# Kernel optimization log

Hardware: AMD Instinct MI355X
Metric: run time of the kernel (lower is better)

Reference implementation:

```python
import jax, jax.numpy as jnp
import numpy as np

N_NODES = 100000
N_EDGES = 4000000
IN_DIM = 3
HID = 8
EPS = 1e-5


def _layer_norm(h, g, b):
    m = jnp.mean(h, axis=-1, keepdims=True)
    v = jnp.mean(jnp.square(h - m), axis=-1, keepdims=True)
    return (h - m) * jax.lax.rsqrt(v + EPS) * g + b


def setup_inputs() -> dict:
    key = jax.random.key(0)
    ks = jax.random.split(key, 10)
    x = jax.random.normal(ks[0], (N_NODES, IN_DIM), dtype=jnp.float32)
    edge_index = jax.random.randint(ks[1], (2, N_EDGES), 0, N_NODES, dtype=jnp.int64)

    def lin(k, fan_in, fan_out):
        bound = 1.0 / np.sqrt(fan_in)
        kw, kb = jax.random.split(k)
        W = jax.random.uniform(kw, (fan_in, fan_out), jnp.float32, -bound, bound)
        b = jax.random.uniform(kb, (fan_out,), jnp.float32, -bound, bound)
        return W, b

    W0, b0 = lin(ks[2], 2 * IN_DIM, HID)
    W1, b1 = lin(ks[3], HID, HID)
    W2, b2 = lin(ks[4], HID, HID)
    W3, b3 = lin(ks[5], HID, 1)
    g0 = jnp.ones((HID,), jnp.float32); be0 = jnp.zeros((HID,), jnp.float32)
    g1 = jnp.ones((HID,), jnp.float32); be1 = jnp.zeros((HID,), jnp.float32)
    g2 = jnp.ones((HID,), jnp.float32); be2 = jnp.zeros((HID,), jnp.float32)
    return {"x": x, "edge_index": edge_index,
            "W0": W0, "b0": b0, "g0": g0, "be0": be0,
            "W1": W1, "b1": b1, "g1": g1, "be1": be1,
            "W2": W2, "b2": b2, "g2": g2, "be2": be2,
            "W3": W3, "b3": b3}


def reference(x, edge_index, W0, b0, g0, be0, W1, b1, g1, be1, W2, b2, g2, be2, W3, b3):
    start, end = edge_index[0], edge_index[1]
    # [E, 2*IN_DIM] gathered edge inputs
    e = jnp.concatenate([x[start], x[end]], axis=1)
    h = jnp.tanh(_layer_norm(e @ W0 + b0, g0, be0))
    h = jnp.tanh(_layer_norm(h @ W1 + b1, g1, be1))
    h = jnp.tanh(_layer_norm(h @ W2 + b2, g2, be2))
    out = (h @ W3 + b3).squeeze(-1)  # [E]
    return out
```

## Files before the change

kernel.cpp:

```cpp
#include <hip/hip_runtime.h>

typedef _Float16 h2 __attribute__((ext_vector_type(2)));
typedef float f4v __attribute__((ext_vector_type(4)));
typedef f4v f4u __attribute__((aligned(4)));

#define N_EDGES 4000000
#define HID 8
#define NPT 4
#define TWO_LOG2E 2.8853900817779268f
#define LN_EPS 1e-5f

#define O_GC0 0
#define O_BC0 8
#define O_GC1 16
#define O_BC1 24
#define O_GC2 32
#define O_BC2 40
#define O_B1  48
#define O_B2  56
#define O_B3  64
#define O_W1P 72
#define O_W2P 104
#define O_W3P 136
#define O_W0C 144
#define O_B0C 192

#if __has_builtin(__builtin_amdgcn_fdot2)
#define FDOT2(a, b, c) __builtin_amdgcn_fdot2((a), (b), (c), false)
#else
#define FDOT2(a, b, c) ((float)(a)[0] * (float)(b)[0] + ((float)(a)[1] * (float)(b)[1] + (c)))
#endif

__global__ void prep_kernel(
    const float* __restrict__ W0, const float* __restrict__ b0,
    const float* __restrict__ g0, const float* __restrict__ be0,
    const float* __restrict__ W1, const float* __restrict__ b1,
    const float* __restrict__ g1, const float* __restrict__ be1,
    const float* __restrict__ W2, const float* __restrict__ b2,
    const float* __restrict__ g2, const float* __restrict__ be2,
    const float* __restrict__ W3, const float* __restrict__ b3,
    float* __restrict__ ws)
{
    if (threadIdx.x != 0) return;
    uint* wsu = reinterpret_cast<uint*>(ws);
    for (int j = 0; j < 8; ++j) {
        ws[O_GC0 + j] = g0[j] * TWO_LOG2E;  ws[O_BC0 + j] = be0[j] * TWO_LOG2E;
        ws[O_GC1 + j] = g1[j] * TWO_LOG2E;  ws[O_BC1 + j] = be1[j] * TWO_LOG2E;
        ws[O_GC2 + j] = g2[j] * TWO_LOG2E;  ws[O_BC2 + j] = be2[j] * TWO_LOG2E;
    }
    {
        float bm = 0.f;
        for (int j = 0; j < 8; ++j) bm += b0[j];
        bm *= 0.125f;
        for (int j = 0; j < 8; ++j) ws[O_B0C + j] = b0[j] - bm;
        for (int k = 0; k < 6; ++k) {
            float rm = 0.f;
            for (int j = 0; j < 8; ++j) rm += W0[k * 8 + j];
            rm *= 0.125f;
            for (int j = 0; j < 8; ++j) ws[O_W0C + k * 8 + j] = W0[k * 8 + j] - rm;
        }
    }
    const float* Ws[2] = {W1, W2};
    const float* bs[2] = {b1, b2};
    const int    wo[2] = {O_W1P, O_W2P};
    const int    bo[2] = {O_B1, O_B2};
    for (int L = 0; L < 2; ++L) {
        const float* W = Ws[L];
        float Wc[64];
        for (int k = 0; k < 8; ++k) {
            float rm = 0.f;
            for (int j = 0; j < 8; ++j) rm += W[k * 8 + j];
            rm *= 0.125f;
            for (int j = 0; j < 8; ++j) Wc[k * 8 + j] = -2.f * (W[k * 8 + j] - rm);
        }
        for (int k = 0; k < 8; ++k) {
            float m = 0.f;
            for (int j = 0; j < 8; ++j) m += (float)(_Float16)Wc[k * 8 + j];
            m *= 0.125f;
            for (int j = 0; j < 8; ++j) Wc[k * 8 + j] -= m;
        }
        for (int j = 0; j < 8; ++j)
            for (int q = 0; q < 4; ++q) {
                h2 v;
                v[0] = (_Float16)Wc[(2 * q) * 8 + j];
                v[1] = (_Float16)Wc[(2 * q + 1) * 8 + j];
                wsu[wo[L] + j * 4 + q] = __builtin_bit_cast(uint, v);
            }
        float mb = 0.f, tot = 0.f;
        for (int j = 0; j < 8; ++j) mb += bs[L][j];
        for (int i = 0; i < 64; ++i) tot += W[i];
        for (int j = 0; j < 8; ++j) {
            float cs = 0.f;
            for (int k = 0; k < 8; ++k) cs += W[k * 8 + j];
            ws[bo[L] + j] = bs[L][j] + cs - mb * 0.125f - tot * 0.125f;
        }
    }
    {
        float s = 0.f;
        for (int k = 0; k < 8; ++k) s += W3[k];
        ws[O_B3] = b3[0] + s;
        for (int q = 0; q < 4; ++q) {
            h2 v;
            v[0] = (_Float16)(-2.f * W3[2 * q]);
            v[1] = (_Float16)(-2.f * W3[2 * q + 1]);
            wsu[O_W3P + q] = __builtin_bit_cast(uint, v);
        }
    }
}

template<int N>
__device__ __forceinline__ void ln_pack(const float (&z)[N][HID],
                                        const float* __restrict__ gc,
                                        const float* __restrict__ bc,
                                        h2 (&p)[N][4]) {
    float r[N];
#pragma unroll
    for (int e = 0; e < N; ++e) {
        float va = 0.f;
#pragma unroll
        for (int j = 0; j < HID; ++j) va = __builtin_fmaf(z[e][j], z[e][j], va);
        r[e] = __builtin_amdgcn_rsqf(__builtin_fmaf(va, 0.125f, LN_EPS));
    }
    float e1[N][HID];
#pragma unroll
    for (int j = 0; j < HID; ++j) {
        const float gcj = gc[j], bcj = bc[j];
#pragma unroll
        for (int e = 0; e < N; ++e) {
            const float y = __builtin_fmaf(z[e][j], r[e] * gcj, bcj);
            e1[e][j] = __builtin_amdgcn_exp2f(y) + 1.0f;
        }
    }
#pragma unroll
    for (int q = 0; q < 4; ++q)
#pragma unroll
        for (int e = 0; e < N; ++e) {
            const float a = e1[e][2 * q], b = e1[e][2 * q + 1];
            const float pr = __builtin_amdgcn_rcpf(a * b);
            p[e][q] = __builtin_bit_cast(h2,
                __builtin_amdgcn_cvt_pkrtz(b * pr, a * pr));
        }
}

template<int N>
__device__ __forceinline__ void lin8_dot(const h2 (&p)[N][4],
                                         const uint* __restrict__ wp,
                                         const float* __restrict__ b,
                                         float (&zo)[N][HID]) {
#pragma unroll
    for (int j = 0; j < HID; ++j) {
        const float bj = b[j];
        const h2 w0 = __builtin_bit_cast(h2, wp[j * 4 + 0]);
        const h2 w1 = __builtin_bit_cast(h2, wp[j * 4 + 1]);
        const h2 w2 = __builtin_bit_cast(h2, wp[j * 4 + 2]);
        const h2 w3 = __builtin_bit_cast(h2, wp[j * 4 + 3]);
#pragma unroll
        for (int e = 0; e < N; ++e) {
            float acc = FDOT2(p[e][0], w0, bj);
            acc = FDOT2(p[e][1], w1, acc);
            acc = FDOT2(p[e][2], w2, acc);
            zo[e][j] = FDOT2(p[e][3], w3, acc);
        }
    }
}

__global__ __launch_bounds__(256) void edge_mlp_kernel(
    const float* __restrict__ x,
    const int*   __restrict__ ei,
    const float* __restrict__ ws,
    float* __restrict__ out)
{
    const int t = blockIdx.x * blockDim.x + threadIdx.x;
    const int base = t * NPT;
    if (base >= N_EDGES) return;

    const uint* wsu = reinterpret_cast<const uint*>(ws);
    const int4 sv = *reinterpret_cast<const int4*>(ei + base);
    const int4 dv = *reinterpret_cast<const int4*>(ei + N_EDGES + base);
    const uint si[NPT] = {(uint)sv.x, (uint)sv.y, (uint)sv.z, (uint)sv.w};
    const uint di[NPT] = {(uint)dv.x, (uint)dv.y, (uint)dv.z, (uint)dv.w};

    f4u vs[NPT], vd[NPT];
#pragma unroll
    for (int e = 0; e < NPT; ++e) {
        vs[e] = *reinterpret_cast<const f4u*>(x + (size_t)(si[e] * 3u));
        vd[e] = *reinterpret_cast<const f4u*>(x + (size_t)(di[e] * 3u));
    }

    float z[NPT][HID];
#pragma unroll
    for (int j = 0; j < HID; ++j) {
        const float w0 = ws[O_W0C + 0 * 8 + j], w1 = ws[O_W0C + 1 * 8 + j],
                    w2 = ws[O_W0C + 2 * 8 + j], w3 = ws[O_W0C + 3 * 8 + j],
                    w4 = ws[O_W0C + 4 * 8 + j], w5 = ws[O_W0C + 5 * 8 + j];
        const float bb = ws[O_B0C + j];
#pragma unroll
        for (int e = 0; e < NPT; ++e) {
            float a = __builtin_fmaf(vs[e][0], w0, bb);
            a = __builtin_fmaf(vs[e][1], w1, a);
            a = __builtin_fmaf(vs[e][2], w2, a);
            a = __builtin_fmaf(vd[e][0], w3, a);
            a = __builtin_fmaf(vd[e][1], w4, a);
            z[e][j] = __builtin_fmaf(vd[e][2], w5, a);
        }
    }

    h2 p[NPT][4];
    ln_pack<NPT>(z, ws + O_GC0, ws + O_BC0, p);
    lin8_dot<NPT>(p, wsu + O_W1P, ws + O_B1, z);
    ln_pack<NPT>(z, ws + O_GC1, ws + O_BC1, p);
    lin8_dot<NPT>(p, wsu + O_W2P, ws + O_B2, z);
    ln_pack<NPT>(z, ws + O_GC2, ws + O_BC2, p);

    const h2 w30 = __builtin_bit_cast(h2, wsu[O_W3P + 0]);
    const h2 w31 = __builtin_bit_cast(h2, wsu[O_W3P + 1]);
    const h2 w32 = __builtin_bit_cast(h2, wsu[O_W3P + 2]);
    const h2 w33 = __builtin_bit_cast(h2, wsu[O_W3P + 3]);
    const float bb3 = ws[O_B3];
    float o[NPT];
#pragma unroll
    for (int e = 0; e < NPT; ++e) {
        float acc = FDOT2(p[e][0], w30, bb3);
        acc = FDOT2(p[e][1], w31, acc);
        acc = FDOT2(p[e][2], w32, acc);
        o[e] = FDOT2(p[e][3], w33, acc);
    }

    *reinterpret_cast<float4*>(out + base) = make_float4(o[0], o[1], o[2], o[3]);
}

extern "C" void kernel_launch(void* const* d_in, const int* in_sizes, int n_in,
                              void* d_out, int out_size, void* d_ws, size_t ws_size,
                              hipStream_t stream) {
    const float* x   = (const float*)d_in[0];
    const int*   ei  = (const int*)d_in[1];
    const float* W0  = (const float*)d_in[2];
    const float* b0  = (const float*)d_in[3];
    const float* g0  = (const float*)d_in[4];
    const float* be0 = (const float*)d_in[5];
    const float* W1  = (const float*)d_in[6];
    const float* b1  = (const float*)d_in[7];
    const float* g1  = (const float*)d_in[8];
    const float* be1 = (const float*)d_in[9];
    const float* W2  = (const float*)d_in[10];
    const float* b2  = (const float*)d_in[11];
    const float* g2  = (const float*)d_in[12];
    const float* be2 = (const float*)d_in[13];
    const float* W3  = (const float*)d_in[14];
    const float* b3  = (const float*)d_in[15];
    float* out = (float*)d_out;
    float* ws  = (float*)d_ws;

    prep_kernel<<<1, 64, 0, stream>>>(W0, b0, g0, be0, W1, b1, g1, be1,
                                      W2, b2, g2, be2, W3, b3, ws);

    const int nthreads = N_EDGES / NPT;
    const int blocks = (nthreads + 255) / 256;
    edge_mlp_kernel<<<blocks, 256, 0, stream>>>(x, ei, ws, out);
}
```

Before: 55.22 us.

## Pack node features to fp16 table and use fdot2 for first layer

The prep kernel now writes a compact 8-byte fp16 copy of each node's features into the workspace, and parallelizes the weight preprocessing across threads. The edge kernel gathers from this packed table instead of 12-16 byte fp32 rows, and computes the first linear layer with fp16 dot2 instructions using packed, zero-padded W0. This is meant to cut gather bandwidth and first-layer ALU work, at the cost of an extra per-call node conversion pass and lower input precision. A fallback path keeps fp32 gathers with conversion when the workspace is too small.

```diff
diff --git a/kernel.cpp b/kernel.cpp
--- a/kernel.cpp
+++ b/kernel.cpp
@@ -1,10 +1,9 @@
 #include <hip/hip_runtime.h>
 
 typedef _Float16 h2 __attribute__((ext_vector_type(2)));
-typedef float f4v __attribute__((ext_vector_type(4)));
-typedef f4v f4u __attribute__((aligned(4)));
 
 #define N_EDGES 4000000
+#define N_NODES 100000
 #define HID 8
 #define NPT 4
 #define TWO_LOG2E 2.8853900817779268f
@@ -22,8 +21,10 @@
 #define O_W1P 72
 #define O_W2P 104
 #define O_W3P 136
-#define O_W0C 144
-#define O_B0C 192
+#define O_W0P 144
+#define O_B0C 176
+#define O_XH  256
+#define WS_FLOATS_NEEDED (256 + 2 * N_NODES)
 
 #if __has_builtin(__builtin_amdgcn_fdot2)
 #define FDOT2(a, b, c) __builtin_amdgcn_fdot2((a), (b), (c), false)
@@ -31,7 +32,42 @@
 #define FDOT2(a, b, c) ((float)(a)[0] * (float)(b)[0] + ((float)(a)[1] * (float)(b)[1] + (c)))
 #endif
 
+__device__ void prep_hidden_layer(const float* __restrict__ W,
+                                  const float* __restrict__ b,
+                                  float* __restrict__ ws, uint* __restrict__ wsu,
+                                  int wofs, int bofs) {
+    float Wc[64];
+    for (int k = 0; k < 8; ++k) {
+        float rm = 0.f;
+        for (int j = 0; j < 8; ++j) rm += W[k * 8 + j];
+        rm *= 0.125f;
+        for (int j = 0; j < 8; ++j) Wc[k * 8 + j] = -2.f * (W[k * 8 + j] - rm);
+    }
+    for (int k = 0; k < 8; ++k) {
+        float m = 0.f;
+        for (int j = 0; j < 8; ++j) m += (float)(_Float16)Wc[k * 8 + j];
+        m *= 0.125f;
+        for (int j = 0; j < 8; ++j) Wc[k * 8 + j] -= m;
+    }
+    for (int j = 0; j < 8; ++j)
+        for (int q = 0; q < 4; ++q) {
+            h2 v;
+            v[0] = (_Float16)Wc[(2 * q) * 8 + j];
+            v[1] = (_Float16)Wc[(2 * q + 1) * 8 + j];
+            wsu[wofs + j * 4 + q] = __builtin_bit_cast(uint, v);
+        }
+    float mb = 0.f, tot = 0.f;
+    for (int j = 0; j < 8; ++j) mb += b[j];
+    for (int i = 0; i < 64; ++i) tot += W[i];
+    for (int j = 0; j < 8; ++j) {
+        float cs = 0.f;
+        for (int k = 0; k < 8; ++k) cs += W[k * 8 + j];
+        ws[bofs + j] = b[j] + cs - mb * 0.125f - tot * 0.125f;
+    }
+}
+
 __global__ void prep_kernel(
+    const float* __restrict__ x,
     const float* __restrict__ W0, const float* __restrict__ b0,
     const float* __restrict__ g0, const float* __restrict__ be0,
     const float* __restrict__ W1, const float* __restrict__ b1,
@@ -39,71 +75,72 @@
     const float* __restrict__ W2, const float* __restrict__ b2,
     const float* __restrict__ g2, const float* __restrict__ be2,
     const float* __restrict__ W3, const float* __restrict__ b3,
-    float* __restrict__ ws)
+    float* __restrict__ ws, int use_tables)
 {
-    if (threadIdx.x != 0) return;
+    const int t = threadIdx.x;
     uint* wsu = reinterpret_cast<uint*>(ws);
-    for (int j = 0; j < 8; ++j) {
-        ws[O_GC0 + j] = g0[j] * TWO_LOG2E;  ws[O_BC0 + j] = be0[j] * TWO_LOG2E;
-        ws[O_GC1 + j] = g1[j] * TWO_LOG2E;  ws[O_BC1 + j] = be1[j] * TWO_LOG2E;
-        ws[O_GC2 + j] = g2[j] * TWO_LOG2E;  ws[O_BC2 + j] = be2[j] * TWO_LOG2E;
-    }
-    {
-        float bm = 0.f;
-        for (int j = 0; j < 8; ++j) bm += b0[j];
-        bm *= 0.125f;
-        for (int j = 0; j < 8; ++j) ws[O_B0C + j] = b0[j] - bm;
-        for (int k = 0; k < 6; ++k) {
-            float rm = 0.f;
-            for (int j = 0; j < 8; ++j) rm += W0[k * 8 + j];
-            rm *= 0.125f;
-            for (int j = 0; j < 8; ++j) ws[O_W0C + k * 8 + j] = W0[k * 8 + j] - rm;
-        }
-    }
-    const float* Ws[2] = {W1, W2};
-    const float* bs[2] = {b1, b2};
-    const int    wo[2] = {O_W1P, O_W2P};
-    const int    bo[2] = {O_B1, O_B2};
-    for (int L = 0; L < 2; ++L) {
-        const float* W = Ws[L];
-        float Wc[64];
-        for (int k = 0; k < 8; ++k) {
-            float rm = 0.f;
-            for (int j = 0; j < 8; ++j) rm += W[k * 8 + j];
-            rm *= 0.125f;
-            for (int j = 0; j < 8; ++j) Wc[k * 8 + j] = -2.f * (W[k * 8 + j] - rm);
-        }
-        for (int k = 0; k < 8; ++k) {
-            float m = 0.f;
-            for (int j = 0; j < 8; ++j) m += (float)(_Float16)Wc[k * 8 + j];
-            m *= 0.125f;
-            for (int j = 0; j < 8; ++j) Wc[k * 8 + j] -= m;
-        }
-        for (int j = 0; j < 8; ++j)
+
+    if (blockIdx.x == 0) {
+        if (t == 0) {
+            for (int j = 0; j < 8; ++j) {
+                ws[O_GC0 + j] = g0[j] * TWO_LOG2E;  ws[O_BC0 + j] = be0[j] * TWO_LOG2E;
+                ws[O_GC1 + j] = g1[j] * TWO_LOG2E;  ws[O_BC1 + j] = be1[j] * TWO_LOG2E;
+                ws[O_GC2 + j] = g2[j] * TWO_LOG2E;  ws[O_BC2 + j] = be2[j] * TWO_LOG2E;
+            }
+        } else if (t == 1) {
+            float Wc[48];
+            for (int k = 0; k < 6; ++k) {
+                float rm = 0.f;
+                for (int j = 0; j < 8; ++j) rm += W0[k * 8 + j];
+                rm *= 0.125f;
+                for (int j = 0; j < 8; ++j) Wc[k * 8 + j] = W0[k * 8 + j] - rm;
+            }
+            for (int k = 0; k < 6; ++k) {
+                float m = 0.f;
+                for (int j = 0; j < 8; ++j) m += (float)(_Float16)Wc[k * 8 + j];
+                m *= 0.125f;
+                for (int j = 0; j < 8; ++j) Wc[k * 8 + j] -= m;
+            }
+            for (int j = 0; j < 8; ++j) {
+                h2 v;
+                v[0] = (_Float16)Wc[0 * 8 + j]; v[1] = (_Float16)Wc[1 * 8 + j];
+                wsu[O_W0P + j * 4 + 0] = __builtin_bit_cast(uint, v);
+                v[0] = (_Float16)Wc[2 * 8 + j]; v[1] = (_Float16)0.f;
+                wsu[O_W0P + j * 4 + 1] = __builtin_bit_cast(uint, v);
+                v[0] = (_Float16)Wc[3 * 8 + j]; v[1] = (_Float16)Wc[4 * 8 + j];
+                wsu[O_W0P + j * 4 + 2] = __builtin_bit_cast(uint, v);
+                v[0] = (_Float16)Wc[5 * 8 + j]; v[1] = (_Float16)0.f;
+                wsu[O_W0P + j * 4 + 3] = __builtin_bit_cast(uint, v);
+            }
+            float bm = 0.f;
+            for (int j = 0; j < 8; ++j) bm += b0[j];
+            bm *= 0.125f;
+            for (int j = 0; j < 8; ++j) ws[O_B0C + j] = b0[j] - bm;
+        } else if (t == 2) {
+            prep_hidden_layer(W1, b1, ws, wsu, O_W1P, O_B1);
+        } else if (t == 3) {
+            prep_hidden_layer(W2, b2, ws, wsu, O_W2P, O_B2);
+        } else if (t == 4) {
+            float s = 0.f;
+            for (int k = 0; k < 8; ++k) s += W3[k];
+            ws[O_B3] = b3[0] + s;
             for (int q = 0; q < 4; ++q) {
                 h2 v;
-                v[0] = (_Float16)Wc[(2 * q) * 8 + j];
-                v[1] = (_Float16)Wc[(2 * q + 1) * 8 + j];
-                wsu[wo[L] + j * 4 + q] = __builtin_bit_cast(uint, v);
-            }
-        float mb = 0.f, tot = 0.f;
-        for (int j = 0; j < 8; ++j) mb += bs[L][j];
-        for (int i = 0; i < 64; ++i) tot += W[i];
-        for (int j = 0; j < 8; ++j) {
-            float cs = 0.f;
-            for (int k = 0; k < 8; ++k) cs += W[k * 8 + j];
-            ws[bo[L] + j] = bs[L][j] + cs - mb * 0.125f - tot * 0.125f;
-        }
-    }
-    {
-        float s = 0.f;
-        for (int k = 0; k < 8; ++k) s += W3[k];
-        ws[O_B3] = b3[0] + s;
-        for (int q = 0; q < 4; ++q) {
-            h2 v;
-            v[0] = (_Float16)(-2.f * W3[2 * q]);
-            v[1] = (_Float16)(-2.f * W3[2 * q + 1]);
-            wsu[O_W3P + q] = __builtin_bit_cast(uint, v);
+                v[0] = (_Float16)(-2.f * W3[2 * q]);
+                v[1] = (_Float16)(-2.f * W3[2 * q + 1]);
+                wsu[O_W3P + q] = __builtin_bit_cast(uint, v);
+            }
+        }
+    }
+
+    if (use_tables) {
+        const int n = blockIdx.x * blockDim.x + t;
+        if (n < N_NODES) {
+            const float x0 = x[n * 3 + 0], x1 = x[n * 3 + 1], x2 = x[n * 3 + 2];
+            uint2 v;
+            v.x = __builtin_bit_cast(uint, __builtin_amdgcn_cvt_pkrtz(x0, x1));
+            v.y = __builtin_bit_cast(uint, __builtin_amdgcn_cvt_pkrtz(x2, 0.f));
+            reinterpret_cast<uint2*>(ws + O_XH)[n] = v;
         }
     }
 }
@@ -164,6 +201,7 @@
     }
 }
 
+template<bool UT>
 __global__ __launch_bounds__(256) void edge_mlp_kernel(
     const float* __restrict__ x,
     const int*   __restrict__ ei,
@@ -180,28 +218,41 @@
     const uint si[NPT] = {(uint)sv.x, (uint)sv.y, (uint)sv.z, (uint)sv.w};
     const uint di[NPT] = {(uint)dv.x, (uint)dv.y, (uint)dv.z, (uint)dv.w};
 
-    f4u vs[NPT], vd[NPT];
+    h2 s01[NPT], s2z[NPT], d01[NPT], d2z[NPT];
 #pragma unroll
     for (int e = 0; e < NPT; ++e) {
-        vs[e] = *reinterpret_cast<const f4u*>(x + (size_t)(si[e] * 3u));
-        vd[e] = *reinterpret_cast<const f4u*>(x + (size_t)(di[e] * 3u));
+        if (UT) {
+            const uint2* XH = reinterpret_cast<const uint2*>(ws + O_XH);
+            const uint2 a = XH[si[e]];
+            const uint2 b = XH[di[e]];
+            s01[e] = __builtin_bit_cast(h2, a.x);
+            s2z[e] = __builtin_bit_cast(h2, a.y);
+            d01[e] = __builtin_bit_cast(h2, b.x);
+            d2z[e] = __builtin_bit_cast(h2, b.y);
+        } else {
+            const float s0 = x[si[e] * 3u], s1 = x[si[e] * 3u + 1], s2 = x[si[e] * 3u + 2];
+            const float d0 = x[di[e] * 3u], d1 = x[di[e] * 3u + 1], d2 = x[di[e] * 3u + 2];
+            s01[e] = __builtin_bit_cast(h2, __builtin_amdgcn_cvt_pkrtz(s0, s1));
+            s2z[e] = __builtin_bit_cast(h2, __builtin_amdgcn_cvt_pkrtz(s2, 0.f));
+            d01[e] = __builtin_bit_cast(h2, __builtin_amdgcn_cvt_pkrtz(d0, d1));
+            d2z[e] = __builtin_bit_cast(h2, __builtin_amdgcn_cvt_pkrtz(d2, 0.f));
+        }
     }
 
     float z[NPT][HID];
 #pragma unroll
     for (int j = 0; j < HID; ++j) {
-        const float w0 = ws[O_W0C + 0 * 8 + j], w1 = ws[O_W0C + 1 * 8 + j],
-                    w2 = ws[O_W0C + 2 * 8 + j], w3 = ws[O_W0C + 3 * 8 + j],
-                    w4 = ws[O_W0C + 4 * 8 + j], w5 = ws[O_W0C + 5 * 8 + j];
+        const h2 wj0 = __builtin_bit_cast(h2, wsu[O_W0P + j * 4 + 0]);
+        const h2 wj1 = __builtin_bit_cast(h2, wsu[O_W0P + j * 4 + 1]);
+        const h2 wj2 = __builtin_bit_cast(h2, wsu[O_W0P + j * 4 + 2]);
+        const h2 wj3 = __builtin_bit_cast(h2, wsu[O_W0P + j * 4 + 3]);
         const float bb = ws[O_B0C + j];
 #pragma unroll
         for (int e = 0; e < NPT; ++e) {
-            float a = __builtin_fmaf(vs[e][0], w0, bb);
-            a = __builtin_fmaf(vs[e][1], w1, a);
-            a = __builtin_fmaf(vs[e][2], w2, a);
-            a = __builtin_fmaf(vd[e][0], w3, a);
-            a = __builtin_fmaf(vd[e][1], w4, a);
-            z[e][j] = __builtin_fmaf(vd[e][2], w5, a);
+            float a = FDOT2(s01[e], wj0, bb);
+            a = FDOT2(s2z[e], wj1, a);
+            a = FDOT2(d01[e], wj2, a);
+            z[e][j] = FDOT2(d2z[e], wj3, a);
         }
     }
 
@@ -251,10 +302,16 @@
     float* out = (float*)d_out;
     float* ws  = (float*)d_ws;
 
-    prep_kernel<<<1, 64, 0, stream>>>(W0, b0, g0, be0, W1, b1, g1, be1,
-                                      W2, b2, g2, be2, W3, b3, ws);
+    const bool ut = ws_size >= (size_t)WS_FLOATS_NEEDED * sizeof(float);
+    const int prep_blocks = ut ? (N_NODES + 255) / 256 : 1;
+    prep_kernel<<<prep_blocks, 256, 0, stream>>>(
+        x, W0, b0, g0, be0, W1, b1, g1, be1, W2, b2, g2, be2, W3, b3,
+        ws, ut ? 1 : 0);
 
     const int nthreads = N_EDGES / NPT;
     const int blocks = (nthreads + 255) / 256;
-    edge_mlp_kernel<<<blocks, 256, 0, stream>>>(x, ei, ws, out);
-}
+    if (ut)
+        edge_mlp_kernel<true><<<blocks, 256, 0, stream>>>(x, ei, ws, out);
+    else
+        edge_mlp_kernel<false><<<blocks, 256, 0, stream>>>(x, ei, ws, out);
+}
```

New measurement: 60.10 us. +8.9%, slower.
